# Kernel tuning notes

Measured on AMD Instinct MI355X. Metric: run time of the kernel, lower is better.

## Reference

```python
import jax, jax.numpy as jnp
import numpy as np

N_ORB = 1024    # Monte-Carlo orbits
NTIMES = 1024   # observation epochs
N_FZ = 24       # zodi flux grid points (uniform in log10)
N_KEZ = 6       # exozodi multipliers (sorted, searchsorted lookup)
N_TINT = 64     # integration times
N_ALPHA = 512   # separations (uniform in log10)


def setup_inputs() -> dict:
    key = jax.random.key(0)
    k1, k2, k3, k4 = jax.random.split(key, 4)
    fZs = jnp.logspace(-10.0, -7.0, N_FZ).astype(jnp.float32)
    alphas = jnp.logspace(-2.0, 1.0, N_ALPHA).astype(jnp.float32)
    kEZs = jnp.array([0.5, 1.0, 2.0, 5.0, 10.0, 20.0], dtype=jnp.float32)
    # grid already in the module's internal (n_fZ, n_kEZ, n_tint, n_alpha) layout
    grid = 25.0 + jax.random.normal(k1, (N_FZ, N_KEZ, N_TINT, N_ALPHA), dtype=jnp.float32)
    # alpha slightly exceeds [alphas[0], alphas[-1]] so geom_mask is exercised
    alpha = (10.0 ** jax.random.uniform(k2, (N_ORB, NTIMES), minval=-2.2, maxval=1.1)).astype(jnp.float32)
    dMag = (25.0 + jax.random.normal(k3, (N_ORB, NTIMES))).astype(jnp.float32)
    fZ_vals = (10.0 ** jax.random.uniform(k4, (NTIMES,), minval=-10.0, maxval=-7.0)).astype(jnp.float32)
    kEZ_val = jnp.float32(1.5)
    return dict(alpha=alpha, dMag=dMag, fZ_vals=fZ_vals, kEZ_val=kEZ_val,
                grid=grid, fZs=fZs, kEZs=kEZs, alphas=alphas)


def reference(alpha, dMag, fZ_vals, kEZ_val, grid, fZs, kEZs, alphas):
    """Faithful vectorized translation of dMag0Grid._pdet_alpha_dMag.

    alpha, dMag: (n_orb, ntimes); fZ_vals: (ntimes,); kEZ_val: scalar;
    grid: (n_fZ, n_kEZ, n_tint, n_alpha). Returns pdet (ntimes, n_tint).
    """
    n_fZ = fZs.shape[0]
    n_alpha = alphas.shape[0]
    log_fZs = jnp.log10(fZs)
    inv_log_fZ_step = 1.0 / (log_fZs[1] - log_fZs[0])
    log_alphas = jnp.log10(alphas)
    inv_log_alpha_step = 1.0 / (log_alphas[1] - log_alphas[0])

    geom_mask = (alpha >= alphas[0]) & (alpha <= alphas[-1])          # (n_orb, ntimes)

    fZ_ind = (jnp.log10(fZ_vals) - log_fZs[0]) * inv_log_fZ_step
    fZ0 = jnp.clip(jnp.floor(fZ_ind).astype(jnp.int32) + 1, 0, n_fZ - 2)  # (ntimes,)

    a_ind = (jnp.log10(alpha) - log_alphas[0]) * inv_log_alpha_step
    a0 = jnp.clip(a_ind.astype(jnp.int32), 0, n_alpha - 1)               # (n_orb, ntimes)
    dalpha = (a_ind - a0).astype(grid.dtype)

    kEZ_ind = jnp.searchsorted(kEZs, kEZ_val, side='right') - 1

    # lax.dynamic_slice clamps the start so the width-2 window fits:
    s = jnp.minimum(a0, n_alpha - 2)                                     # (n_orb, ntimes)

    g = jnp.take(grid, kEZ_ind, axis=1)                                  # (n_fZ, n_tint, n_alpha)
    g_f = g[fZ0]                                                          # (ntimes, n_tint, n_alpha)
    sT = s.T                                                              # (ntimes, n_orb)
    g0 = jnp.take_along_axis(g_f, sT[:, None, :], axis=2)                 # (ntimes, n_tint, n_orb)
    g1 = jnp.take_along_axis(g_f, (sT + 1)[:, None, :], axis=2)
    res = g0 + dalpha.T[:, None, :] * (g1 - g0)                           # (ntimes, n_tint, n_orb)

    dim = jnp.transpose(res, (2, 0, 1))                                   # (n_orb, ntimes, n_tint)
    det_mask = geom_mask[..., None] & jnp.signbit(dMag[..., None] - dim)
    pdet = det_mask.astype(jnp.float32).mean(axis=0)                      # (ntimes, n_tint)
    return pdet
```

## Files before the change

kernel.cpp:

```cpp
#include <hip/hip_runtime.h>
#include <math.h>

#define N_ORB   1024
#define NTIMES  1024
#define N_FZ    24
#define N_KEZ   6
#define N_TINT  64
#define N_ALPHA 512

#define GT_BYTES (N_FZ * N_ALPHA * N_TINT * 4)

__global__ __launch_bounds__(256) void stage_inputs(
    const float* __restrict__ grid, const float* __restrict__ kEZs,
    const float* __restrict__ kEZ_val_p, const float* __restrict__ alpha,
    const float* __restrict__ dMag, const float* __restrict__ alphas,
    float* __restrict__ gT, float4* __restrict__ P)
{
    __shared__ float lds[64 * 65];

    int b = blockIdx.x;
    if (b < 192) {
        float kv = kEZ_val_p[0];
        int cnt = 0;
#pragma unroll
        for (int i = 0; i < N_KEZ; ++i) cnt += (kEZs[i] <= kv) ? 1 : 0;
        int kez = cnt - 1;
        kez = kez < 0 ? 0 : (kez > N_KEZ - 1 ? N_KEZ - 1 : kez);

        int fz = b >> 3, sc = b & 7;
        int w = threadIdx.x >> 6, lane = threadIdx.x & 63;
        const float* gsrc = grid + ((size_t)fz * N_KEZ + kez) * N_TINT * N_ALPHA;

#pragma unroll
        for (int r = 0; r < 16; ++r) {
            int tint = w * 16 + r;
            lds[tint * 65 + lane] = gsrc[(size_t)tint * N_ALPHA + sc * 64 + lane];
        }
        __syncthreads();
#pragma unroll
        for (int r = 0; r < 16; ++r) {
            int sl = w * 16 + r;
            gT[((size_t)fz * N_ALPHA + sc * 64 + sl) * N_TINT + lane] = lds[lane * 65 + sl];
        }
    } else {
        float* da = lds;
        float* dm = lds + 1056;
        int*   of = (int*)(lds + 2112);

        int u = b - 192;
        int t0 = (u & 31) * 32, o0 = (u >> 5) * 32;
        int row = threadIdx.x >> 5, col = threadIdx.x & 31;

        float al0 = alphas[0], al1 = alphas[N_ALPHA - 1];
        float la0 = log10f(al0);
        float inv_step = 1.0f / (log10f(alphas[1]) - la0);

#pragma unroll
        for (int r = 0; r < 4; ++r) {
            int ol = r * 8 + row;
            size_t idx = (size_t)(o0 + ol) * NTIMES + t0 + col;
            float a = alpha[idx];
            float d = dMag[idx];
            float a_ind = (log10f(a) - la0) * inv_step;
            int a0i = (int)a_ind;
            a0i = a0i < 0 ? 0 : (a0i > N_ALPHA - 1 ? N_ALPHA - 1 : a0i);
            float dal = a_ind - (float)a0i;
            int s = a0i > N_ALPHA - 2 ? N_ALPHA - 2 : a0i;
            bool geom = (a >= al0) && (a <= al1);
            da[ol * 33 + col] = dal;
            dm[ol * 33 + col] = geom ? d : __builtin_inff();
            of[ol * 33 + col] = s * N_TINT;
        }
        __syncthreads();
#pragma unroll
        for (int r = 0; r < 4; ++r) {
            int tl = r * 8 + row;
            float4 v;
            v.x = da[col * 33 + tl];
            v.y = dm[col * 33 + tl];
            v.z = __int_as_float(of[col * 33 + tl]);
            v.w = 0.0f;
            P[(size_t)(t0 + tl) * N_ORB + o0 + col] = v;
        }
    }
}

__global__ __launch_bounds__(256) void pdet_main(
    const float* __restrict__ fZ_vals, const float* __restrict__ fZs,
    const float* __restrict__ gT, const float4* __restrict__ P,
    float* __restrict__ out)
{
    __shared__ float4 Psort[N_ORB];
    __shared__ int    hist[512];
    __shared__ int    histPS[512];
    __shared__ int    red[4 * 64];

    int t = blockIdx.x;
    int tid = threadIdx.x;
    int w = tid >> 6, lane = tid & 63;

    float lf0 = log10f(fZs[0]);
    float inv_f = 1.0f / (log10f(fZs[1]) - lf0);
    float fi = (log10f(fZ_vals[t]) - lf0) * inv_f;
    int f0 = (int)floorf(fi) + 1;
    f0 = f0 < 0 ? 0 : (f0 > N_FZ - 2 ? N_FZ - 2 : f0);

    const float*  gB = gT + (size_t)f0 * N_ALPHA * N_TINT;
    const float4* Pt = P + (size_t)t * N_ORB;

    hist[tid] = 0; hist[tid + 256] = 0;
    __syncthreads();

    float4 v[4];
    int    bin[4];
#pragma unroll
    for (int k = 0; k < 4; ++k) {
        v[k] = Pt[tid + k * 256];
        int s = __float_as_int(v[k].z) >> 6;
        bin[k] = isinf(v[k].y) ? 511 : s;
        atomicAdd(&hist[bin[k]], 1);
    }
    __syncthreads();

    if (tid < 64) {
        int pre[8]; int run = 0;
#pragma unroll
        for (int j = 0; j < 8; ++j) { pre[j] = run; run += hist[tid * 8 + j]; }
        int inc = run;
#pragma unroll
        for (int d = 1; d < 64; d <<= 1) {
            int n = __shfl_up(inc, d);
            if (lane >= d) inc += n;
        }
        int excl = inc - run;
#pragma unroll
        for (int j = 0; j < 8; ++j) histPS[tid * 8 + j] = excl + pre[j];
    }
    __syncthreads();

#pragma unroll
    for (int k = 0; k < 4; ++k) {
        int pos = atomicAdd(&histPS[bin[k]], 1);
        Psort[pos] = v[k];
    }
    __syncthreads();

    int q  = lane >> 4;
    int tg = (lane & 15) << 2;
    int base = w * 256;

    int c0 = 0, c1 = 0, c2 = 0, c3 = 0;

#pragma unroll 4
    for (int it = 0; it < 64; ++it) {
        float4 pd = Psort[base + it * 4 + q];
        float dal = pd.x, dm = pd.y;
        int offw = __float_as_int(pd.z);
        const float4* rowp = reinterpret_cast<const float4*>(gB + offw + tg);
        float4 g0 = rowp[0];
        float4 g1 = rowp[16];
        c0 += dm < fmaf(dal, g1.x - g0.x, g0.x);
        c1 += dm < fmaf(dal, g1.y - g0.y, g0.y);
        c2 += dm < fmaf(dal, g1.z - g0.z, g0.z);
        c3 += dm < fmaf(dal, g1.w - g0.w, g0.w);
    }

    c0 += __shfl_xor(c0, 16); c0 += __shfl_xor(c0, 32);
    c1 += __shfl_xor(c1, 16); c1 += __shfl_xor(c1, 32);
    c2 += __shfl_xor(c2, 16); c2 += __shfl_xor(c2, 32);
    c3 += __shfl_xor(c3, 16); c3 += __shfl_xor(c3, 32);

    if (lane < 16) {
        red[w * 64 + lane * 4 + 0] = c0;
        red[w * 64 + lane * 4 + 1] = c1;
        red[w * 64 + lane * 4 + 2] = c2;
        red[w * 64 + lane * 4 + 3] = c3;
    }
    __syncthreads();
    if (tid < 64) {
        int tot = red[tid] + red[64 + tid] + red[128 + tid] + red[192 + tid];
        out[(size_t)t * N_TINT + tid] = (float)tot * (1.0f / 1024.0f);
    }
}

extern "C" void kernel_launch(void* const* d_in, const int* in_sizes, int n_in,
                              void* d_out, int out_size, void* d_ws, size_t ws_size,
                              hipStream_t stream) {
    const float* alpha   = (const float*)d_in[0];
    const float* dMag    = (const float*)d_in[1];
    const float* fZ_vals = (const float*)d_in[2];
    const float* kEZ_val = (const float*)d_in[3];
    const float* grid    = (const float*)d_in[4];
    const float* fZs     = (const float*)d_in[5];
    const float* kEZs    = (const float*)d_in[6];
    const float* alphas  = (const float*)d_in[7];
    float*  out = (float*)d_out;

    float*  gT = (float*)d_ws;
    float4* P  = (float4*)((char*)d_ws + GT_BYTES);

    stage_inputs<<<dim3(192 + 1024), 256, 0, stream>>>(
        grid, kEZs, kEZ_val, alpha, dMag, alphas, gT, P);
    pdet_main<<<dim3(NTIMES), 256, 0, stream>>>(fZ_vals, fZs, gT, P, out);
}
```

Before: 104.2 us.

## Pack per-orbit params into float2 and reuse grid rows across sorted bins

Each orbit's alpha index and fraction are folded into one float, so the staged record shrinks from float4 to float2, halving the intermediate buffer and its LDS footprint. The main loop now gives each lane one tint column and walks the bin-sorted orbits sequentially, reloading grid rows only when the wave-uniform bin changes and reusing the previous upper row when bins are adjacent. Out-of-range orbits get u=0 and an infinite dMag, so they never count. This trades the earlier 4-orbits-per-wave gather for a serial, branchy loop with a chain of dependent loads, and refolding the index into a float may change the interpolation fraction slightly.

```diff
diff --git a/kernel.cpp b/kernel.cpp
--- a/kernel.cpp
+++ b/kernel.cpp
@@ -14,7 +14,7 @@
     const float* __restrict__ grid, const float* __restrict__ kEZs,
     const float* __restrict__ kEZ_val_p, const float* __restrict__ alpha,
     const float* __restrict__ dMag, const float* __restrict__ alphas,
-    float* __restrict__ gT, float4* __restrict__ P)
+    float* __restrict__ gT, float2* __restrict__ Pc)
 {
     __shared__ float lds[64 * 65];
 
@@ -43,9 +43,8 @@
             gT[((size_t)fz * N_ALPHA + sc * 64 + sl) * N_TINT + lane] = lds[lane * 65 + sl];
         }
     } else {
-        float* da = lds;
-        float* dm = lds + 1056;
-        int*   of = (int*)(lds + 2112);
+        float* ut = lds;
+        float* dt = lds + 1056;
 
         int u = b - 192;
         int t0 = (u & 31) * 32, o0 = (u >> 5) * 32;
@@ -67,30 +66,30 @@
             float dal = a_ind - (float)a0i;
             int s = a0i > N_ALPHA - 2 ? N_ALPHA - 2 : a0i;
             bool geom = (a >= al0) && (a <= al1);
-            da[ol * 33 + col] = dal;
-            dm[ol * 33 + col] = geom ? d : __builtin_inff();
-            of[ol * 33 + col] = s * N_TINT;
+            float uv = (float)s + dal;
+            uv = fminf(fmaxf(uv, 0.0f), 510.999f);
+            if (!geom) uv = 0.0f;
+            ut[ol * 33 + col] = uv;
+            dt[ol * 33 + col] = geom ? d : __builtin_inff();
         }
         __syncthreads();
 #pragma unroll
         for (int r = 0; r < 4; ++r) {
             int tl = r * 8 + row;
-            float4 v;
-            v.x = da[col * 33 + tl];
-            v.y = dm[col * 33 + tl];
-            v.z = __int_as_float(of[col * 33 + tl]);
-            v.w = 0.0f;
-            P[(size_t)(t0 + tl) * N_ORB + o0 + col] = v;
+            float2 v;
+            v.x = ut[col * 33 + tl];
+            v.y = dt[col * 33 + tl];
+            Pc[(size_t)(t0 + tl) * N_ORB + o0 + col] = v;
         }
     }
 }
 
 __global__ __launch_bounds__(256) void pdet_main(
     const float* __restrict__ fZ_vals, const float* __restrict__ fZs,
-    const float* __restrict__ gT, const float4* __restrict__ P,
+    const float* __restrict__ gT, const float2* __restrict__ Pc,
     float* __restrict__ out)
 {
-    __shared__ float4 Psort[N_ORB];
+    __shared__ float2 Psort[N_ORB];
     __shared__ int    hist[512];
     __shared__ int    histPS[512];
     __shared__ int    red[4 * 64];
@@ -106,18 +105,18 @@
     f0 = f0 < 0 ? 0 : (f0 > N_FZ - 2 ? N_FZ - 2 : f0);
 
     const float*  gB = gT + (size_t)f0 * N_ALPHA * N_TINT;
-    const float4* Pt = P + (size_t)t * N_ORB;
+    const float2* Pt = Pc + (size_t)t * N_ORB;
 
     hist[tid] = 0; hist[tid + 256] = 0;
     __syncthreads();
 
-    float4 v[4];
+    float2 v[4];
     int    bin[4];
 #pragma unroll
     for (int k = 0; k < 4; ++k) {
         v[k] = Pt[tid + k * 256];
-        int s = __float_as_int(v[k].z) >> 6;
-        bin[k] = isinf(v[k].y) ? 511 : s;
+        int s = (int)v[k].x;
+        bin[k] = s > 510 ? 510 : s;
         atomicAdd(&hist[bin[k]], 1);
     }
     __syncthreads();
@@ -145,37 +144,33 @@
     }
     __syncthreads();
 
-    int q  = lane >> 4;
-    int tg = (lane & 15) << 2;
     int base = w * 256;
-
-    int c0 = 0, c1 = 0, c2 = 0, c3 = 0;
-
-#pragma unroll 4
-    for (int it = 0; it < 64; ++it) {
-        float4 pd = Psort[base + it * 4 + q];
-        float dal = pd.x, dm = pd.y;
-        int offw = __float_as_int(pd.z);
-        const float4* rowp = reinterpret_cast<const float4*>(gB + offw + tg);
-        float4 g0 = rowp[0];
-        float4 g1 = rowp[16];
-        c0 += dm < fmaf(dal, g1.x - g0.x, g0.x);
-        c1 += dm < fmaf(dal, g1.y - g0.y, g0.y);
-        c2 += dm < fmaf(dal, g1.z - g0.z, g0.z);
-        c3 += dm < fmaf(dal, g1.w - g0.w, g0.w);
-    }
-
-    c0 += __shfl_xor(c0, 16); c0 += __shfl_xor(c0, 32);
-    c1 += __shfl_xor(c1, 16); c1 += __shfl_xor(c1, 32);
-    c2 += __shfl_xor(c2, 16); c2 += __shfl_xor(c2, 32);
-    c3 += __shfl_xor(c3, 16); c3 += __shfl_xor(c3, 32);
-
-    if (lane < 16) {
-        red[w * 64 + lane * 4 + 0] = c0;
-        red[w * 64 + lane * 4 + 1] = c1;
-        red[w * 64 + lane * 4 + 2] = c2;
-        red[w * 64 + lane * 4 + 3] = c3;
-    }
+    int cnt = 0;
+    float g0 = 0.0f, g1 = 0.0f, dg = 0.0f;
+    int cur = -2;
+
+    for (int ib = 0; ib < 64; ++ib) {
+        float2 p0 = Psort[base + ib * 4 + 0];
+        float2 p1 = Psort[base + ib * 4 + 1];
+        float2 p2 = Psort[base + ib * 4 + 2];
+        float2 p3 = Psort[base + ib * 4 + 3];
+#pragma unroll
+        for (int j = 0; j < 4; ++j) {
+            float2 p = j == 0 ? p0 : (j == 1 ? p1 : (j == 2 ? p2 : p3));
+            float u = p.x, dm = p.y;
+            int su = __builtin_amdgcn_readfirstlane((int)u);
+            if (su != cur) {
+                if (su != cur + 1) g0 = gB[su * N_TINT + lane];
+                else               g0 = g1;
+                g1 = gB[su * N_TINT + N_TINT + lane];
+                dg = g1 - g0;
+                cur = su;
+            }
+            cnt += dm < fmaf(u - (float)su, dg, g0);
+        }
+    }
+
+    red[w * 64 + lane] = cnt;
     __syncthreads();
     if (tid < 64) {
         int tot = red[tid] + red[64 + tid] + red[128 + tid] + red[192 + tid];
@@ -197,9 +192,9 @@
     float*  out = (float*)d_out;
 
     float*  gT = (float*)d_ws;
-    float4* P  = (float4*)((char*)d_ws + GT_BYTES);
+    float2* Pc = (float2*)((char*)d_ws + GT_BYTES);
 
     stage_inputs<<<dim3(192 + 1024), 256, 0, stream>>>(
-        grid, kEZs, kEZ_val, alpha, dMag, alphas, gT, P);
-    pdet_main<<<dim3(NTIMES), 256, 0, stream>>>(fZ_vals, fZs, gT, P, out);
+        grid, kEZs, kEZ_val, alpha, dMag, alphas, gT, Pc);
+    pdet_main<<<dim3(NTIMES), 256, 0, stream>>>(fZ_vals, fZs, gT, Pc, out);
 }
```

Result: slower. 136.8 us (+31.2%).
